# Kernel optimization log

Hardware: AMD Instinct MI355X
Metric: run time of the kernel (lower is better)

## Reference

```python
import jax, jax.numpy as jnp
import numpy as np

E = 1024      # embed_dim
QH = 16       # query heads
KVH = 4       # kv heads
HD = E // QH  # head_dim = 64
KVE = HD * KVH  # 256
EPS = 1e-5
ROPE_BASE = 10000.0


def rope(x, d):
    # Faithful to the source RoPE: d == number of heads (x.shape[-2]),
    # and the 'sequence' axis of the cache is x.shape[0] (the batch dim).
    # rope(x) = x*cos + (x*sin) * neg_half(x)  (note: nonlinear in x).
    b = x.shape[0]
    theta = 1.0 / (ROPE_BASE ** (jnp.arange(0, d, 2, dtype=jnp.float32) / d))  # (d//2,)
    seq_idx = jnp.arange(b, dtype=jnp.float32)                                 # (b,)
    idx_theta = seq_idx[:, None] * theta[None, :]                              # (b, d//2)
    idx2 = jnp.concatenate([idx_theta, idx_theta], axis=-1)                    # (b, d)
    # cached shape (b,1,1,d); source permutes (0,1,3,2) -> (b,1,d,1)
    cos = jnp.cos(idx2)[:, None, :, None]  # (b,1,d,1)
    sin = jnp.sin(idx2)[:, None, :, None]
    d2 = d // 2
    # split of the LAST dim (head_dim) at d//2 == num_heads//2, as in source
    neg = jnp.concatenate([-x[..., d2:], x[..., :d2]], axis=-1)
    return x * cos + (x * sin) * neg


def setup_inputs() -> dict:
    key = jax.random.key(0)
    ks = jax.random.split(key, 12)
    b, n = 1, 2048

    def xavier(k, shape):
        fan_out, fan_in = shape
        std = (2.0 / (fan_in + fan_out)) ** 0.5
        return jax.random.normal(k, shape, dtype=jnp.float32) * std

    return {
        "query": jax.random.normal(ks[0], (b, n, E), dtype=jnp.float32),
        "key": jax.random.normal(ks[1], (b, n, E), dtype=jnp.float32),
        "value": jax.random.normal(ks[2], (b, n, E), dtype=jnp.float32),
        "Wq": xavier(ks[3], (E, E)),
        "bq": jnp.zeros((E,), jnp.float32),
        "Wk": xavier(ks[4], (KVE, E)),
        "bk": jnp.zeros((KVE,), jnp.float32),
        "Wv": xavier(ks[5], (KVE, E)),
        "bv": jnp.zeros((KVE,), jnp.float32),
        "gamma": jnp.ones((E,), jnp.float32),
        "beta": jnp.zeros((E,), jnp.float32),
    }


def reference(query, key, value, Wq, bq, Wk, bk, Wv, bv, gamma, beta):
    b, n, _ = query.shape
    q = query @ Wq.T + bq            # (b,n,E)
    k = key @ Wk.T + bk              # (b,n,KVE)
    v = value @ Wv.T + bv            # (b,n,KVE)

    q = q.reshape(b, n, QH, HD)      # b n h d
    k = k.reshape(b, n, KVH, HD)
    v = v.reshape(b, n, KVH, HD)

    q = rope(q, QH)
    k = rope(k, KVH)

    # b n h d -> b h n d
    q = jnp.transpose(q, (0, 2, 1, 3))
    k = jnp.transpose(k, (0, 2, 1, 3))
    v = jnp.transpose(v, (0, 2, 1, 3))

    scale = float(HD) ** 0.5
    q = q / scale

    g = QH // KVH
    # 'b (h g) n d -> b g h n d' : h outer, g inner
    q = q.reshape(b, KVH, g, n, HD)              # (b, h, g, n, d)
    q = jnp.transpose(q, (0, 2, 1, 3, 4))        # (b, g, h, n, d)

    sim = jnp.einsum('bghnd,bhsd->bghns', q, k)  # (b,g,h,n,s)
    attn = jax.nn.softmax(sim, axis=-1)
    out = jnp.einsum('bghns,bhsd->bghnd', attn, v)

    # 'b g h n d -> b n (h g) d'
    out = jnp.transpose(out, (0, 3, 2, 1, 4))    # (b, n, h, g, d)
    x = out.reshape(b, n, QH * HD)               # (b, n, E)

    # LayerNorm (biased variance, as in torch)
    mu = jnp.mean(x, axis=-1, keepdims=True)
    var = jnp.mean((x - mu) ** 2, axis=-1, keepdims=True)
    x = (x - mu) * jax.lax.rsqrt(var + EPS) * gamma + beta

    # NOTE: source computes out_proj(x) but returns x, so out_proj is dead code.
    return x
```

## Files before the change

### kernel.cpp

```cpp
#include <hip/hip_runtime.h>
#include <math.h>

#define EDIM   1024
#define KVEDIM 256
#define HDIM   64
#define QHEADS 16

typedef __attribute__((ext_vector_type(8))) short short8;
typedef __attribute__((ext_vector_type(4))) float f32x4;

__device__ __forceinline__ unsigned pack2(float a, float b) {
    unsigned ua = __builtin_bit_cast(unsigned, a);
    unsigned ub = __builtin_bit_cast(unsigned, b);
    ua += 0x7fffu + ((ua >> 16) & 1u);
    ub += 0x7fffu + ((ub >> 16) & 1u);
    return (ua >> 16) | (ub & 0xffff0000u);
}
__device__ __forceinline__ short f2b(float a) {
    unsigned ua = __builtin_bit_cast(unsigned, a);
    ua += 0x7fffu + ((ua >> 16) & 1u);
    return (short)(ua >> 16);
}

__global__ __launch_bounds__(256)
void cvt_bf16(const float* __restrict__ s0, const float* __restrict__ s1,
              const float* __restrict__ s2, const float* __restrict__ s3,
              const float* __restrict__ s4, const float* __restrict__ s5,
              short* __restrict__ d0, short* __restrict__ d1,
              short* __restrict__ d2, short* __restrict__ d3,
              short* __restrict__ d4, short* __restrict__ d5,
              int n0, int n1, int n2, int n3, int n4, int n5)
{
    const float* s; short* d; int n;
    switch (blockIdx.y) {
        case 0: s = s0; d = d0; n = n0; break;
        case 1: s = s1; d = d1; n = n1; break;
        case 2: s = s2; d = d2; n = n2; break;
        case 3: s = s3; d = d3; n = n3; break;
        case 4: s = s4; d = d4; n = n4; break;
        default: s = s5; d = d5; n = n5; break;
    }
    int i = ((int)blockIdx.x * 256 + threadIdx.x) * 8;
    if (i >= n) return;
    float4 a = *(const float4*)&s[i];
    float4 b = *(const float4*)&s[i + 4];
    uint4 o;
    o.x = pack2(a.x, a.y); o.y = pack2(a.z, a.w);
    o.z = pack2(b.x, b.y); o.w = pack2(b.z, b.w);
    *(uint4*)&d[i] = o;
}

__global__ __launch_bounds__(256)
void proj_gemm(const short* __restrict__ Aq, const short* __restrict__ Ak,
               const short* __restrict__ Av,
               const short* __restrict__ Wqb, const short* __restrict__ Wkb,
               const short* __restrict__ Wvb,
               const float* __restrict__ bq, const float* __restrict__ bk,
               const float* __restrict__ bv,
               short* __restrict__ Cq, short* __restrict__ Ck,
               short* __restrict__ Cv, float qscale)
{
    const int bid = blockIdx.x;
    const short* A; const short* W; const float* bias; short* C;
    int N, bm, bn; float scale;
    if (bid < 128) {
        A = Aq; W = Wqb; bias = bq; C = Cq; N = EDIM; scale = qscale;
        bm = (bid >> 3) * 128; bn = (bid & 7) * 128;
    } else if (bid < 160) {
        int i = bid - 128;
        A = Ak; W = Wkb; bias = bk; C = Ck; N = KVEDIM; scale = 1.0f;
        bm = (i >> 1) * 128; bn = (i & 1) * 128;
    } else {
        int i = bid - 160;
        A = Av; W = Wvb; bias = bv; C = Cv; N = KVEDIM; scale = 1.0f;
        bm = (i >> 1) * 128; bn = (i & 1) * 128;
    }
    const int K = EDIM;

    __shared__ short As[128 * 72];
    __shared__ short Ws[128 * 72];

    const int t = threadIdx.x, lane = t & 63, wv = t >> 6;
    const int lm = lane & 15, quad = lane >> 4;
    const int q8 = quad * 8, q4 = quad * 4;
    const int wm = (wv & 1) * 64, wn = (wv >> 1) * 64;
    const int sr = t >> 3, sc = (t & 7) * 8;

    f32x4 zero = {0.f, 0.f, 0.f, 0.f};
    f32x4 acc[4][4];
    #pragma unroll
    for (int i = 0; i < 4; ++i)
        #pragma unroll
        for (int j = 0; j < 4; ++j) acc[i][j] = zero;

    for (int k0 = 0; k0 < K; k0 += 64) {
        __syncthreads();
        #pragma unroll
        for (int i = 0; i < 4; ++i) {
            int r = sr + i * 32;
            *(uint4*)&As[r * 72 + sc] = *(const uint4*)&A[(size_t)(bm + r) * K + k0 + sc];
            *(uint4*)&Ws[r * 72 + sc] = *(const uint4*)&W[(size_t)(bn + r) * K + k0 + sc];
        }
        __syncthreads();
        #pragma unroll
        for (int ks = 0; ks < 2; ++ks) {
            short8 af[4], bfr[4];
            #pragma unroll
            for (int i = 0; i < 4; ++i)
                af[i] = *(const short8*)&As[(wm + i * 16 + lm) * 72 + ks * 32 + q8];
            #pragma unroll
            for (int j = 0; j < 4; ++j)
                bfr[j] = *(const short8*)&Ws[(wn + j * 16 + lm) * 72 + ks * 32 + q8];
            #pragma unroll
            for (int i = 0; i < 4; ++i)
                #pragma unroll
                for (int j = 0; j < 4; ++j)
                    acc[i][j] = __builtin_amdgcn_mfma_f32_16x16x32_bf16(
                        af[i], bfr[j], acc[i][j], 0, 0, 0);
        }
    }

    #pragma unroll
    for (int j = 0; j < 4; ++j) {
        float bj = bias[bn + wn + j * 16 + lm];
        #pragma unroll
        for (int i = 0; i < 4; ++i)
            #pragma unroll
            for (int r = 0; r < 4; ++r)
                C[(size_t)(bm + wm + i * 16 + q4 + r) * N + bn + wn + j * 16 + lm] =
                    f2b((acc[i][j][r] + bj) * scale);
    }
}

__global__ __launch_bounds__(256)
void attn_mfma(const short* __restrict__ q, const short* __restrict__ k,
               const short* __restrict__ v, float* __restrict__ x, int n)
{
    __shared__ short Ks[64 * 72];
    __shared__ short Vt[64 * 72];
    __shared__ short Ps[64 * 72];
    __shared__ float Lred[4][64];

    const int qh = blockIdx.y, kvh = qh >> 2;
    const int r0 = blockIdx.x * 64;
    const int t = threadIdx.x;
    const int lane = t & 63, wv = t >> 6;
    const int lm = lane & 15, quad = lane >> 4;
    const int q8 = quad * 8, q4 = quad * 4;

    short8 qf[4][2];
    #pragma unroll
    for (int qt = 0; qt < 4; ++qt) {
        const short* qrow = &q[(size_t)(r0 + qt * 16 + lm) * EDIM + qh * HDIM];
        qf[qt][0] = *(const short8*)&qrow[q8];
        qf[qt][1] = *(const short8*)&qrow[32 + q8];
    }

    const int rt0 = (wv & 1) * 2;
    const int dt0 = (wv >> 1) * 2;

    f32x4 zero = {0.f, 0.f, 0.f, 0.f};
    f32x4 oacc[2][2];
    #pragma unroll
    for (int i = 0; i < 2; ++i)
        #pragma unroll
        for (int j = 0; j < 2; ++j) oacc[i][j] = zero;
    float lp[4] = {0.f, 0.f, 0.f, 0.f};

    const int krow = t >> 2, kc = (t & 3) * 8;
    const int vs4 = (t & 15) * 4, vd0 = (t >> 4) * 4;

    for (int s0 = 0; s0 < n; s0 += 64) {
        __syncthreads();
        {
            const uint4* ksrc = (const uint4*)&k[(size_t)(s0 + krow) * KVEDIM + kvh * HDIM];
            uint4 ka = ksrc[t & 3];
            uint4 kb = ksrc[(t & 3) + 4];
            *(uint4*)&Ks[krow * 72 + kc] = ka;
            *(uint4*)&Ks[krow * 72 + kc + 32] = kb;
        }
        {
            unsigned vr[4][2];
            #pragma unroll
            for (int i = 0; i < 4; ++i) {
                uint2 vv = *(const uint2*)&v[(size_t)(s0 + vs4 + i) * KVEDIM + kvh * HDIM + vd0];
                vr[i][0] = vv.x; vr[i][1] = vv.y;
            }
            #pragma unroll
            for (int j = 0; j < 4; ++j) {
                int w = j >> 1, hi = (j & 1) * 16;
                unsigned e0 = (vr[0][w] >> hi) & 0xffffu;
                unsigned e1 = (vr[1][w] >> hi) & 0xffffu;
                unsigned e2 = (vr[2][w] >> hi) & 0xffffu;
                unsigned e3 = (vr[3][w] >> hi) & 0xffffu;
                uint2 o; o.x = e0 | (e1 << 16); o.y = e2 | (e3 << 16);
                *(uint2*)&Vt[(vd0 + j) * 72 + vs4] = o;
            }
        }
        __syncthreads();

        short8 kf0 = *(const short8*)&Ks[(wv * 16 + lm) * 72 + q8];
        short8 kf1 = *(const short8*)&Ks[(wv * 16 + lm) * 72 + 32 + q8];
        #pragma unroll
        for (int qt = 0; qt < 4; ++qt) {
            f32x4 s = zero;
            s = __builtin_amdgcn_mfma_f32_16x16x32_bf16(kf0, qf[qt][0], s, 0, 0, 0);
            s = __builtin_amdgcn_mfma_f32_16x16x32_bf16(kf1, qf[qt][1], s, 0, 0, 0);
            float p0 = exp2f(s[0]);
            float p1 = exp2f(s[1]);
            float p2 = exp2f(s[2]);
            float p3 = exp2f(s[3]);
            lp[qt] += (p0 + p1) + (p2 + p3);
            uint2 pw; pw.x = pack2(p0, p1); pw.y = pack2(p2, p3);
            *(uint2*)&Ps[(qt * 16 + lm) * 72 + wv * 16 + q4] = pw;
        }
        __syncthreads();

        short8 vf[2][2];
        #pragma unroll
        for (int j = 0; j < 2; ++j) {
            vf[j][0] = *(const short8*)&Vt[((dt0 + j) * 16 + lm) * 72 + q8];
            vf[j][1] = *(const short8*)&Vt[((dt0 + j) * 16 + lm) * 72 + 32 + q8];
        }
        #pragma unroll
        for (int i = 0; i < 2; ++i) {
            short8 pf0 = *(const short8*)&Ps[((rt0 + i) * 16 + lm) * 72 + q8];
            short8 pf1 = *(const short8*)&Ps[((rt0 + i) * 16 + lm) * 72 + 32 + q8];
            #pragma unroll
            for (int j = 0; j < 2; ++j) {
                oacc[i][j] = __builtin_amdgcn_mfma_f32_16x16x32_bf16(pf0, vf[j][0], oacc[i][j], 0, 0, 0);
                oacc[i][j] = __builtin_amdgcn_mfma_f32_16x16x32_bf16(pf1, vf[j][1], oacc[i][j], 0, 0, 0);
            }
        }
    }

    #pragma unroll
    for (int qt = 0; qt < 4; ++qt) {
        float l = lp[qt];
        l += __shfl_xor(l, 16);
        l += __shfl_xor(l, 32);
        if (lane < 16) Lred[wv][qt * 16 + lm] = l;
    }
    __syncthreads();

    #pragma unroll
    for (int i = 0; i < 2; ++i) {
        #pragma unroll
        for (int r = 0; r < 4; ++r) {
            int row = (rt0 + i) * 16 + q4 + r;
            float lsum = (Lred[0][row] + Lred[1][row]) + (Lred[2][row] + Lred[3][row]);
            float inv = 1.0f / lsum;
            #pragma unroll
            for (int j = 0; j < 2; ++j)
                x[(size_t)(r0 + row) * EDIM + qh * HDIM + (dt0 + j) * 16 + lm] =
                    oacc[i][j][r] * inv;
        }
    }
}

__global__ __launch_bounds__(256)
void ln_kernel(float* __restrict__ x, const float* __restrict__ gamma,
               const float* __restrict__ beta)
{
    const int rowbase = (int)blockIdx.x * EDIM;
    const int t = threadIdx.x;

    float4 xv = *(const float4*)&x[rowbase + t * 4];
    float s  = xv.x + xv.y + xv.z + xv.w;
    float sq = xv.x * xv.x + xv.y * xv.y + xv.z * xv.z + xv.w * xv.w;
    #pragma unroll
    for (int m = 1; m < 64; m <<= 1) {
        s  += __shfl_xor(s,  m);
        sq += __shfl_xor(sq, m);
    }
    __shared__ float ws_[4], wq_[4];
    const int wave = t >> 6;
    if ((t & 63) == 0) { ws_[wave] = s; wq_[wave] = sq; }
    __syncthreads();
    s  = ws_[0] + ws_[1] + ws_[2] + ws_[3];
    sq = wq_[0] + wq_[1] + wq_[2] + wq_[3];

    const float mu   = s * (1.f / EDIM);
    const float var  = sq * (1.f / EDIM) - mu * mu;
    const float rstd = rsqrtf(var + 1e-5f);

    float4 g = *(const float4*)&gamma[t * 4];
    float4 b = *(const float4*)&beta[t * 4];
    float4 o;
    o.x = (xv.x - mu) * rstd * g.x + b.x;
    o.y = (xv.y - mu) * rstd * g.y + b.y;
    o.z = (xv.z - mu) * rstd * g.z + b.z;
    o.w = (xv.w - mu) * rstd * g.w + b.w;
    *(float4*)&x[rowbase + t * 4] = o;
}

extern "C" void kernel_launch(void* const* d_in, const int* in_sizes, int n_in,
                              void* d_out, int out_size, void* d_ws, size_t ws_size,
                              hipStream_t stream)
{
    const float* query = (const float*)d_in[0];
    const float* key   = (const float*)d_in[1];
    const float* value = (const float*)d_in[2];
    const float* Wq    = (const float*)d_in[3];
    const float* bq    = (const float*)d_in[4];
    const float* Wk    = (const float*)d_in[5];
    const float* bk    = (const float*)d_in[6];
    const float* Wv    = (const float*)d_in[7];
    const float* bv    = (const float*)d_in[8];
    const float* gamma = (const float*)d_in[9];
    const float* beta  = (const float*)d_in[10];
    float* out = (float*)d_out;

    const int n = in_sizes[0] / EDIM;

    short* qa  = (short*)d_ws;
    short* ka  = qa  + (size_t)n * EDIM;
    short* va  = ka  + (size_t)n * EDIM;
    short* wqb = va  + (size_t)n * EDIM;
    short* wkb = wqb + (size_t)EDIM * EDIM;
    short* wvb = wkb + (size_t)KVEDIM * EDIM;
    short* qb  = wvb + (size_t)KVEDIM * EDIM;
    short* kb  = qb  + (size_t)n * EDIM;
    short* vb  = kb  + (size_t)n * KVEDIM;

    const float qscale = 0.125f * 1.44269504088896f;

    cvt_bf16<<<dim3(1024, 6), 256, 0, stream>>>(
        query, key, value, Wq, Wk, Wv,
        qa, ka, va, wqb, wkb, wvb,
        n * EDIM, n * EDIM, n * EDIM, EDIM * EDIM, KVEDIM * EDIM, KVEDIM * EDIM);

    proj_gemm<<<dim3(192), 256, 0, stream>>>(
        qa, ka, va, wqb, wkb, wvb, bq, bk, bv, qb, kb, vb, qscale);

    attn_mfma<<<dim3(n / 64, QHEADS), 256, 0, stream>>>(qb, kb, vb, out, n);

    ln_kernel<<<dim3(n), 256, 0, stream>>>(out, gamma, beta);
}
```

Measured before the change: 176.1 us.

## Fuse bf16 conversion into projection GEMM, split attention keys, fuse combine with LayerNorm

Drops the separate fp32-to-bf16 conversion kernel. The projection GEMM now loads fp32 inputs and packs them to bf16 while filling shared memory, using smaller 64x64 tiles so more blocks are launched. Attention splits the key range into two segments along a new grid axis and writes unnormalized partial outputs and row sums. A combined kernel merges the partials, normalizes them and applies LayerNorm. This adds fp32 partial-output traffic and redundant weight conversion per tile, in exchange for one fewer launch and more parallelism in attention. The exp2 call is also switched to the hardware builtin.

```diff
diff --git a/kernel.cpp b/kernel.cpp
--- a/kernel.cpp
+++ b/kernel.cpp
@@ -5,6 +5,7 @@
 #define KVEDIM 256
 #define HDIM   64
 #define QHEADS 16
+#define NSEG   2
 
 typedef __attribute__((ext_vector_type(8))) short short8;
 typedef __attribute__((ext_vector_type(4))) float f32x4;
@@ -22,109 +23,92 @@
     return (short)(ua >> 16);
 }
 
+#if __has_builtin(__builtin_amdgcn_exp2f)
+__device__ __forceinline__ float fexp2(float x) { return __builtin_amdgcn_exp2f(x); }
+#else
+__device__ __forceinline__ float fexp2(float x) { return exp2f(x); }
+#endif
+
 __global__ __launch_bounds__(256)
-void cvt_bf16(const float* __restrict__ s0, const float* __restrict__ s1,
-              const float* __restrict__ s2, const float* __restrict__ s3,
-              const float* __restrict__ s4, const float* __restrict__ s5,
-              short* __restrict__ d0, short* __restrict__ d1,
-              short* __restrict__ d2, short* __restrict__ d3,
-              short* __restrict__ d4, short* __restrict__ d5,
-              int n0, int n1, int n2, int n3, int n4, int n5)
-{
-    const float* s; short* d; int n;
-    switch (blockIdx.y) {
-        case 0: s = s0; d = d0; n = n0; break;
-        case 1: s = s1; d = d1; n = n1; break;
-        case 2: s = s2; d = d2; n = n2; break;
-        case 3: s = s3; d = d3; n = n3; break;
-        case 4: s = s4; d = d4; n = n4; break;
-        default: s = s5; d = d5; n = n5; break;
-    }
-    int i = ((int)blockIdx.x * 256 + threadIdx.x) * 8;
-    if (i >= n) return;
-    float4 a = *(const float4*)&s[i];
-    float4 b = *(const float4*)&s[i + 4];
-    uint4 o;
-    o.x = pack2(a.x, a.y); o.y = pack2(a.z, a.w);
-    o.z = pack2(b.x, b.y); o.w = pack2(b.z, b.w);
-    *(uint4*)&d[i] = o;
-}
-
-__global__ __launch_bounds__(256)
-void proj_gemm(const short* __restrict__ Aq, const short* __restrict__ Ak,
-               const short* __restrict__ Av,
-               const short* __restrict__ Wqb, const short* __restrict__ Wkb,
-               const short* __restrict__ Wvb,
+void proj_gemm(const float* __restrict__ Aq, const float* __restrict__ Ak,
+               const float* __restrict__ Av,
+               const float* __restrict__ Wq, const float* __restrict__ Wk,
+               const float* __restrict__ Wv,
                const float* __restrict__ bq, const float* __restrict__ bk,
                const float* __restrict__ bv,
                short* __restrict__ Cq, short* __restrict__ Ck,
                short* __restrict__ Cv, float qscale)
 {
     const int bid = blockIdx.x;
-    const short* A; const short* W; const float* bias; short* C;
+    const float* A; const float* W; const float* bias; short* C;
     int N, bm, bn; float scale;
-    if (bid < 128) {
-        A = Aq; W = Wqb; bias = bq; C = Cq; N = EDIM; scale = qscale;
-        bm = (bid >> 3) * 128; bn = (bid & 7) * 128;
-    } else if (bid < 160) {
-        int i = bid - 128;
-        A = Ak; W = Wkb; bias = bk; C = Ck; N = KVEDIM; scale = 1.0f;
-        bm = (i >> 1) * 128; bn = (i & 1) * 128;
+    if (bid < 512) {
+        A = Aq; W = Wq; bias = bq; C = Cq; N = EDIM; scale = qscale;
+        bm = (bid >> 4) * 64; bn = (bid & 15) * 64;
+    } else if (bid < 640) {
+        int i = bid - 512;
+        A = Ak; W = Wk; bias = bk; C = Ck; N = KVEDIM; scale = 1.0f;
+        bm = (i >> 2) * 64; bn = (i & 3) * 64;
     } else {
-        int i = bid - 160;
-        A = Av; W = Wvb; bias = bv; C = Cv; N = KVEDIM; scale = 1.0f;
-        bm = (i >> 1) * 128; bn = (i & 1) * 128;
+        int i = bid - 640;
+        A = Av; W = Wv; bias = bv; C = Cv; N = KVEDIM; scale = 1.0f;
+        bm = (i >> 2) * 64; bn = (i & 3) * 64;
     }
     const int K = EDIM;
 
-    __shared__ short As[128 * 72];
-    __shared__ short Ws[128 * 72];
+    __shared__ short As[64 * 136];
+    __shared__ short Ws[64 * 136];
 
     const int t = threadIdx.x, lane = t & 63, wv = t >> 6;
     const int lm = lane & 15, quad = lane >> 4;
     const int q8 = quad * 8, q4 = quad * 4;
-    const int wm = (wv & 1) * 64, wn = (wv >> 1) * 64;
-    const int sr = t >> 3, sc = (t & 7) * 8;
+    const int wm = (wv & 1) * 32, wn = (wv >> 1) * 32;
+    const int srow = t >> 5;
+    const int scol = (t & 31) * 4;
 
     f32x4 zero = {0.f, 0.f, 0.f, 0.f};
-    f32x4 acc[4][4];
-    #pragma unroll
-    for (int i = 0; i < 4; ++i)
-        #pragma unroll
-        for (int j = 0; j < 4; ++j) acc[i][j] = zero;
-
-    for (int k0 = 0; k0 < K; k0 += 64) {
-        __syncthreads();
-        #pragma unroll
-        for (int i = 0; i < 4; ++i) {
-            int r = sr + i * 32;
-            *(uint4*)&As[r * 72 + sc] = *(const uint4*)&A[(size_t)(bm + r) * K + k0 + sc];
-            *(uint4*)&Ws[r * 72 + sc] = *(const uint4*)&W[(size_t)(bn + r) * K + k0 + sc];
-        }
-        __syncthreads();
-        #pragma unroll
-        for (int ks = 0; ks < 2; ++ks) {
-            short8 af[4], bfr[4];
-            #pragma unroll
-            for (int i = 0; i < 4; ++i)
-                af[i] = *(const short8*)&As[(wm + i * 16 + lm) * 72 + ks * 32 + q8];
-            #pragma unroll
-            for (int j = 0; j < 4; ++j)
-                bfr[j] = *(const short8*)&Ws[(wn + j * 16 + lm) * 72 + ks * 32 + q8];
-            #pragma unroll
-            for (int i = 0; i < 4; ++i)
+    f32x4 acc[2][2];
+    #pragma unroll
+    for (int i = 0; i < 2; ++i)
+        #pragma unroll
+        for (int j = 0; j < 2; ++j) acc[i][j] = zero;
+
+    for (int k0 = 0; k0 < K; k0 += 128) {
+        __syncthreads();
+        #pragma unroll
+        for (int i = 0; i < 8; ++i) {
+            int r = i * 8 + srow;
+            float4 a = *(const float4*)&A[(size_t)(bm + r) * K + k0 + scol];
+            uint2 pa; pa.x = pack2(a.x, a.y); pa.y = pack2(a.z, a.w);
+            *(uint2*)&As[r * 136 + scol] = pa;
+            float4 w = *(const float4*)&W[(size_t)(bn + r) * K + k0 + scol];
+            uint2 pw; pw.x = pack2(w.x, w.y); pw.y = pack2(w.z, w.w);
+            *(uint2*)&Ws[r * 136 + scol] = pw;
+        }
+        __syncthreads();
+        #pragma unroll
+        for (int ks = 0; ks < 4; ++ks) {
+            short8 af[2], wf[2];
+            #pragma unroll
+            for (int i = 0; i < 2; ++i)
+                af[i] = *(const short8*)&As[(wm + i * 16 + lm) * 136 + ks * 32 + q8];
+            #pragma unroll
+            for (int j = 0; j < 2; ++j)
+                wf[j] = *(const short8*)&Ws[(wn + j * 16 + lm) * 136 + ks * 32 + q8];
+            #pragma unroll
+            for (int i = 0; i < 2; ++i)
                 #pragma unroll
-                for (int j = 0; j < 4; ++j)
+                for (int j = 0; j < 2; ++j)
                     acc[i][j] = __builtin_amdgcn_mfma_f32_16x16x32_bf16(
-                        af[i], bfr[j], acc[i][j], 0, 0, 0);
-        }
-    }
-
-    #pragma unroll
-    for (int j = 0; j < 4; ++j) {
+                        af[i], wf[j], acc[i][j], 0, 0, 0);
+        }
+    }
+
+    #pragma unroll
+    for (int j = 0; j < 2; ++j) {
         float bj = bias[bn + wn + j * 16 + lm];
         #pragma unroll
-        for (int i = 0; i < 4; ++i)
+        for (int i = 0; i < 2; ++i)
             #pragma unroll
             for (int r = 0; r < 4; ++r)
                 C[(size_t)(bm + wm + i * 16 + q4 + r) * N + bn + wn + j * 16 + lm] =
@@ -134,7 +118,8 @@
 
 __global__ __launch_bounds__(256)
 void attn_mfma(const short* __restrict__ q, const short* __restrict__ k,
-               const short* __restrict__ v, float* __restrict__ x, int n)
+               const short* __restrict__ v, float* __restrict__ Opart,
+               float* __restrict__ Lpart, int n)
 {
     __shared__ short Ks[64 * 72];
     __shared__ short Vt[64 * 72];
@@ -143,6 +128,9 @@
 
     const int qh = blockIdx.y, kvh = qh >> 2;
     const int r0 = blockIdx.x * 64;
+    const int seg = blockIdx.z;
+    const int segkeys = n / NSEG;
+    const int sbeg = seg * segkeys;
     const int t = threadIdx.x;
     const int lane = t & 63, wv = t >> 6;
     const int lm = lane & 15, quad = lane >> 4;
@@ -170,7 +158,8 @@
     const int krow = t >> 2, kc = (t & 3) * 8;
     const int vs4 = (t & 15) * 4, vd0 = (t >> 4) * 4;
 
-    for (int s0 = 0; s0 < n; s0 += 64) {
+    for (int c = 0; c < segkeys; c += 64) {
+        const int s0 = sbeg + c;
         __syncthreads();
         {
             const uint4* ksrc = (const uint4*)&k[(size_t)(s0 + krow) * KVEDIM + kvh * HDIM];
@@ -206,10 +195,10 @@
             f32x4 s = zero;
             s = __builtin_amdgcn_mfma_f32_16x16x32_bf16(kf0, qf[qt][0], s, 0, 0, 0);
             s = __builtin_amdgcn_mfma_f32_16x16x32_bf16(kf1, qf[qt][1], s, 0, 0, 0);
-            float p0 = exp2f(s[0]);
-            float p1 = exp2f(s[1]);
-            float p2 = exp2f(s[2]);
-            float p3 = exp2f(s[3]);
+            float p0 = fexp2(s[0]);
+            float p1 = fexp2(s[1]);
+            float p2 = fexp2(s[2]);
+            float p3 = fexp2(s[3]);
             lp[qt] += (p0 + p1) + (p2 + p3);
             uint2 pw; pw.x = pack2(p0, p1); pw.y = pack2(p2, p3);
             *(uint2*)&Ps[(qt * 16 + lm) * 72 + wv * 16 + q4] = pw;
@@ -249,25 +238,46 @@
         for (int r = 0; r < 4; ++r) {
             int row = (rt0 + i) * 16 + q4 + r;
             float lsum = (Lred[0][row] + Lred[1][row]) + (Lred[2][row] + Lred[3][row]);
-            float inv = 1.0f / lsum;
+            if (dt0 == 0 && lm == 0)
+                Lpart[((size_t)seg * n + r0 + row) * QHEADS + qh] = lsum;
             #pragma unroll
             for (int j = 0; j < 2; ++j)
-                x[(size_t)(r0 + row) * EDIM + qh * HDIM + (dt0 + j) * 16 + lm] =
-                    oacc[i][j][r] * inv;
+                Opart[((size_t)seg * n + r0 + row) * EDIM + qh * HDIM + (dt0 + j) * 16 + lm] =
+                    oacc[i][j][r];
         }
     }
 }
 
 __global__ __launch_bounds__(256)
-void ln_kernel(float* __restrict__ x, const float* __restrict__ gamma,
-               const float* __restrict__ beta)
+void combine_ln(const float* __restrict__ Opart, const float* __restrict__ Lpart,
+                const float* __restrict__ gamma, const float* __restrict__ beta,
+                float* __restrict__ out, int n)
 {
-    const int rowbase = (int)blockIdx.x * EDIM;
+    const int r = blockIdx.x;
     const int t = threadIdx.x;
 
-    float4 xv = *(const float4*)&x[rowbase + t * 4];
-    float s  = xv.x + xv.y + xv.z + xv.w;
-    float sq = xv.x * xv.x + xv.y * xv.y + xv.z * xv.z + xv.w * xv.w;
+    __shared__ float linv[QHEADS];
+    if (t < QHEADS) {
+        float l = 0.f;
+        #pragma unroll
+        for (int s = 0; s < NSEG; ++s)
+            l += Lpart[((size_t)s * n + r) * QHEADS + t];
+        linv[t] = 1.0f / l;
+    }
+    __syncthreads();
+
+    const int c = t * 4;
+    float4 o = {0.f, 0.f, 0.f, 0.f};
+    #pragma unroll
+    for (int s = 0; s < NSEG; ++s) {
+        float4 p = *(const float4*)&Opart[((size_t)s * n + r) * EDIM + c];
+        o.x += p.x; o.y += p.y; o.z += p.z; o.w += p.w;
+    }
+    const float inv = linv[c >> 6];
+    o.x *= inv; o.y *= inv; o.z *= inv; o.w *= inv;
+
+    float s  = o.x + o.y + o.z + o.w;
+    float sq = o.x * o.x + o.y * o.y + o.z * o.z + o.w * o.w;
     #pragma unroll
     for (int m = 1; m < 64; m <<= 1) {
         s  += __shfl_xor(s,  m);
@@ -284,14 +294,14 @@
     const float var  = sq * (1.f / EDIM) - mu * mu;
     const float rstd = rsqrtf(var + 1e-5f);
 
-    float4 g = *(const float4*)&gamma[t * 4];
-    float4 b = *(const float4*)&beta[t * 4];
-    float4 o;
-    o.x = (xv.x - mu) * rstd * g.x + b.x;
-    o.y = (xv.y - mu) * rstd * g.y + b.y;
-    o.z = (xv.z - mu) * rstd * g.z + b.z;
-    o.w = (xv.w - mu) * rstd * g.w + b.w;
-    *(float4*)&x[rowbase + t * 4] = o;
+    float4 g = *(const float4*)&gamma[c];
+    float4 b = *(const float4*)&beta[c];
+    float4 y;
+    y.x = (o.x - mu) * rstd * g.x + b.x;
+    y.y = (o.y - mu) * rstd * g.y + b.y;
+    y.z = (o.z - mu) * rstd * g.z + b.z;
+    y.w = (o.w - mu) * rstd * g.w + b.w;
+    *(float4*)&out[(size_t)r * EDIM + c] = y;
 }
 
 extern "C" void kernel_launch(void* const* d_in, const int* in_sizes, int n_in,
@@ -313,27 +323,19 @@
 
     const int n = in_sizes[0] / EDIM;
 
-    short* qa  = (short*)d_ws;
-    short* ka  = qa  + (size_t)n * EDIM;
-    short* va  = ka  + (size_t)n * EDIM;
-    short* wqb = va  + (size_t)n * EDIM;
-    short* wkb = wqb + (size_t)EDIM * EDIM;
-    short* wvb = wkb + (size_t)KVEDIM * EDIM;
-    short* qb  = wvb + (size_t)KVEDIM * EDIM;
-    short* kb  = qb  + (size_t)n * EDIM;
-    short* vb  = kb  + (size_t)n * KVEDIM;
+    short* qb = (short*)d_ws;
+    short* kb = qb + (size_t)n * EDIM;
+    short* vb = kb + (size_t)n * KVEDIM;
+    float* Opart = (float*)(vb + (size_t)n * KVEDIM);
+    float* Lpart = Opart + (size_t)NSEG * n * EDIM;
 
     const float qscale = 0.125f * 1.44269504088896f;
 
-    cvt_bf16<<<dim3(1024, 6), 256, 0, stream>>>(
-        query, key, value, Wq, Wk, Wv,
-        qa, ka, va, wqb, wkb, wvb,
-        n * EDIM, n * EDIM, n * EDIM, EDIM * EDIM, KVEDIM * EDIM, KVEDIM * EDIM);
-
-    proj_gemm<<<dim3(192), 256, 0, stream>>>(
-        qa, ka, va, wqb, wkb, wvb, bq, bk, bv, qb, kb, vb, qscale);
-
-    attn_mfma<<<dim3(n / 64, QHEADS), 256, 0, stream>>>(qb, kb, vb, out, n);
-
-    ln_kernel<<<dim3(n), 256, 0, stream>>>(out, gamma, beta);
-}
+    proj_gemm<<<dim3(768), 256, 0, stream>>>(
+        query, key, value, Wq, Wk, Wv, bq, bk, bv, qb, kb, vb, qscale);
+
+    attn_mfma<<<dim3(n / 64, QHEADS, NSEG), 256, 0, stream>>>(
+        qb, kb, vb, Opart, Lpart, n);
+
+    combine_ln<<<dim3(n), 256, 0, stream>>>(Opart, Lpart, gamma, beta, out, n);
+}
```

New measurement: 188.1 us. 1.07x slower.
